# Optimization experiments

Measured on AMD Instinct MI355X. Metric: run time of the kernel, lower is better.

The kernel has to match this reference:

```python
import jax, jax.numpy as jnp
import numpy as np

N_NODES = 50000
N_EDGES = 800000
IN_CH = 128
CH = 128
OUT_CH = 128
N_TAPS = 3
N_LAYERS = 2


def setup_inputs() -> dict:
    key = jax.random.key(0)
    ks = jax.random.split(key, 8)
    s = 0.05
    x = jax.random.normal(ks[0], (N_NODES, IN_CH), dtype=jnp.float32)
    edge_index = jax.random.randint(ks[1], (2, N_EDGES), 0, N_NODES)
    # readin MLP: 1 layer, plain_last=False -> Linear + activation
    w_in = jax.random.normal(ks[2], (IN_CH, CH), dtype=jnp.float32) * s
    b_in = jnp.zeros((CH,), jnp.float32)
    # per-layer GraphFilter taps: (n_taps+1) Linears of [CH, CH]
    taps_w = jax.random.normal(ks[3], (N_LAYERS, N_TAPS + 1, CH, CH), dtype=jnp.float32) * s
    taps_b = jax.random.normal(ks[4], (N_LAYERS, N_TAPS + 1, CH), dtype=jnp.float32) * s
    # readout MLP: 1 layer, plain_last=True -> Linear only
    w_out = jax.random.normal(ks[5], (CH, OUT_CH), dtype=jnp.float32) * s
    b_out = jnp.zeros((OUT_CH,), jnp.float32)
    return {
        "x": x,
        "edge_index": edge_index,
        "w_in": w_in,
        "b_in": b_in,
        "taps_w": taps_w,
        "taps_b": taps_b,
        "w_out": w_out,
        "b_out": b_out,
    }


def reference(x, edge_index, w_in, b_in, taps_w, taps_b, w_out, b_out):
    act = jax.nn.leaky_relu  # torch LeakyReLU default negative_slope=0.01
    src, dst = edge_index[0], edge_index[1]
    n = x.shape[0]

    # readin: Linear + act (plain_last=False)
    h = act(x @ w_in + b_in)

    n_layers, n_taps_p1 = taps_w.shape[0], taps_w.shape[1]
    for l in range(n_layers):
        # ResidualBlock: y = act(h); y = GraphFilter(y); h = h + y
        y = act(h)
        out = y @ taps_w[l, 0] + taps_b[l, 0]
        for k in range(1, n_taps_p1):
            # SimpleConv(aggr='sum'): y_i = sum_{(s->i) in E} y_s
            y = jax.ops.segment_sum(y[src], dst, num_segments=n)
            out = out + y @ taps_w[l, k] + taps_b[l, k]
        h = h + out

    # readout: Linear only (plain_last=True)
    return h @ w_out + b_out
```

## Files before the change

### kernel.cpp

```cpp
#include <hip/hip_runtime.h>

typedef unsigned int uint;
typedef unsigned short ushort;

using bf16x8 = __attribute__((ext_vector_type(8))) short;
using f32x4  = __attribute__((ext_vector_type(4))) float;
using u32x4  = __attribute__((ext_vector_type(4))) uint;

__device__ __forceinline__ float lrelu(float v) { return v > 0.f ? v : 0.01f * v; }
__device__ __forceinline__ float b2f(ushort u) { return __uint_as_float((uint)u << 16); }
__device__ __forceinline__ ushort f2b(float f) {
  uint u = __float_as_uint(f);
  u += 0x7fffu + ((u >> 16) & 1u);
  return (ushort)(u >> 16);
}

#define CSR_B 256
#define BKT_SHIFT 10
#define MAX_NB 64


template <int MODE, int K, int F32A>
__global__ __launch_bounds__(256) void gemm_mfma(
    const ushort* __restrict__ A0, const ushort* __restrict__ A1,
    const ushort* __restrict__ A2, const ushort* __restrict__ A3,
    const float* __restrict__ Xf,
    const ushort* __restrict__ Wt, const float* __restrict__ bias,
    float* __restrict__ h, ushort* __restrict__ yout, int do_act, int store_h,
    int N) {
  __shared__ ushort As[64][40];
  __shared__ ushort Bs[128][40];
  const int tid = threadIdx.x;
  const int lane = tid & 63;
  const int wave = tid >> 6;
  const int g = lane >> 4;
  const int mr = lane & 15;
  const int wr = wave >> 1;
  const int wc = wave & 1;
  const int row0 = blockIdx.x * 64;

  const ushort* Ap[4] = {A0, A1, A2, A3};

  f32x4 acc[2][4];
#pragma unroll
  for (int i = 0; i < 2; i++)
#pragma unroll
    for (int j = 0; j < 4; j++) acc[i][j] = (f32x4){0.f, 0.f, 0.f, 0.f};

#pragma unroll 4
  for (int kc = 0; kc < K; kc += 32) {
    {
      int m = tid >> 2, q = tid & 3;
      int r = row0 + m;
      if (r >= N) r = N - 1;
      if constexpr (F32A) {
        const float* xp = Xf + (size_t)r * 128 + kc + q * 8;
        f32x4 xa = *(const f32x4*)xp;
        f32x4 xb = *(const f32x4*)(xp + 4);
        union { u32x4 v; ushort u[8]; } o;
        o.u[0] = f2b(xa[0]); o.u[1] = f2b(xa[1]);
        o.u[2] = f2b(xa[2]); o.u[3] = f2b(xa[3]);
        o.u[4] = f2b(xb[0]); o.u[5] = f2b(xb[1]);
        o.u[6] = f2b(xb[2]); o.u[7] = f2b(xb[3]);
        *(u32x4*)&As[m][q * 8] = o.v;
      } else {
        int kg = kc + q * 8;
        const ushort* ap = Ap[kg >> 7] + ((size_t)((kg >> 6) & 1)) * N * 64 +
                           (size_t)r * 64 + (kg & 63);
        *(u32x4*)&As[m][q * 8] = *(const u32x4*)ap;
      }
    }
#pragma unroll
    for (int t = 0; t < 2; t++) {
      int slot = tid + t * 256;
      int n = slot >> 2, q = slot & 3;
      *(u32x4*)&Bs[n][q * 8] = *(const u32x4*)(Wt + (size_t)n * K + kc + q * 8);
    }
    __syncthreads();
    bf16x8 af[2], bf[4];
#pragma unroll
    for (int rt = 0; rt < 2; rt++) af[rt] = *(bf16x8*)&As[wr * 32 + rt * 16 + mr][g * 8];
#pragma unroll
    for (int ct = 0; ct < 4; ct++) bf[ct] = *(bf16x8*)&Bs[wc * 64 + ct * 16 + mr][g * 8];
#pragma unroll
    for (int rt = 0; rt < 2; rt++)
#pragma unroll
      for (int ct = 0; ct < 4; ct++)
        acc[rt][ct] = __builtin_amdgcn_mfma_f32_16x16x32_bf16(af[rt], bf[ct], acc[rt][ct], 0, 0, 0);
    __syncthreads();
  }

#pragma unroll
  for (int rt = 0; rt < 2; rt++) {
#pragma unroll
    for (int i = 0; i < 4; i++) {
      int R = row0 + wr * 32 + rt * 16 + g * 4 + i;
      if (R >= N) continue;
#pragma unroll
      for (int ct = 0; ct < 4; ct++) {
        int c = wc * 64 + ct * 16 + mr;
        float v = acc[rt][ct][i] + bias[c];
        size_t o = (size_t)R * 128 + c;
        size_t oy = (size_t)(c >> 6) * N * 64 + (size_t)R * 64 + (c & 63);
        if (MODE == 0) {
          float hv = lrelu(v);
          h[o] = hv;
          yout[oy] = f2b(lrelu(hv));
        } else if (MODE == 1) {
          float hv = h[o] + v;
          if (store_h) h[o] = hv;
          if (yout) yout[oy] = f2b(do_act ? lrelu(hv) : hv);
        } else {
          h[o] = v;
        }
      }
    }
  }
}

__global__ __launch_bounds__(256) void agg_bf16(const ushort* __restrict__ yin,
                                                ushort* __restrict__ yout,
                                                const int* __restrict__ rowp,
                                                const ushort* __restrict__ esrc, int N) {
  int t = threadIdx.x;
  int chunk = blockIdx.x & 1;
  int node = (blockIdx.x >> 1) * 32 + (t >> 3);
  if (node >= N) return;
  int lane = t & 7;
  const ushort* yb = yin + (size_t)chunk * N * 64 + lane * 8;
  int beg = rowp[node], end = rowp[node + 1];
  float s[8] = {0.f, 0.f, 0.f, 0.f, 0.f, 0.f, 0.f, 0.f};
  int j = beg;
  for (; j + 8 <= end; j += 8) {
    int is[8];
#pragma unroll
    for (int e = 0; e < 8; e++) is[e] = esrc[j + e];
    u32x4 w[8];
#pragma unroll
    for (int e = 0; e < 8; e++) w[e] = *(const u32x4*)(yb + (size_t)is[e] * 64);
#pragma unroll
    for (int e = 0; e < 8; e++) {
      union { u32x4 v; ushort u[8]; } q;
      q.v = w[e];
#pragma unroll
      for (int c = 0; c < 8; c++) s[c] += b2f(q.u[c]);
    }
  }
  if (j + 4 <= end) {
    int is[4];
#pragma unroll
    for (int e = 0; e < 4; e++) is[e] = esrc[j + e];
    u32x4 w[4];
#pragma unroll
    for (int e = 0; e < 4; e++) w[e] = *(const u32x4*)(yb + (size_t)is[e] * 64);
#pragma unroll
    for (int e = 0; e < 4; e++) {
      union { u32x4 v; ushort u[8]; } q;
      q.v = w[e];
#pragma unroll
      for (int c = 0; c < 8; c++) s[c] += b2f(q.u[c]);
    }
    j += 4;
  }
  for (; j < end; j++) {
    int sn = esrc[j];
    union { u32x4 v; ushort u[8]; } w;
    w.v = *(const u32x4*)(yb + (size_t)sn * 64);
#pragma unroll
    for (int e = 0; e < 8; e++) s[e] += b2f(w.u[e]);
  }
  union { u32x4 v; ushort u[8]; } o;
#pragma unroll
  for (int e = 0; e < 8; e++) o.u[e] = f2b(s[e]);
  *(u32x4*)(yout + (size_t)chunk * N * 64 + (size_t)node * 64 + lane * 8) = o.v;
}

__global__ __launch_bounds__(256) void prep_k(const float* __restrict__ w_in,
                                              const float* __restrict__ w_out,
                                              const float* __restrict__ taps_w,
                                              const float* __restrict__ taps_b,
                                              ushort* __restrict__ Wt_in,
                                              ushort* __restrict__ Wt_out,
                                              ushort* __restrict__ Wt_l0,
                                              ushort* __restrict__ Wt_l1,
                                              float* __restrict__ bsum) {
  int gid = blockIdx.x * 256 + threadIdx.x;
  if (gid < 16384) {
    int n = gid >> 7, k = gid & 127;
    Wt_in[gid] = f2b(w_in[k * 128 + n]);
  } else if (gid < 32768) {
    int i = gid - 16384;
    int n = i >> 7, k = i & 127;
    Wt_out[i] = f2b(w_out[k * 128 + n]);
  } else if (gid < 98304) {
    int i = gid - 32768;
    int n = i >> 9, k = i & 511;
    Wt_l0[i] = f2b(taps_w[(size_t)k * 128 + n]);
  } else if (gid < 163840) {
    int i = gid - 98304;
    int n = i >> 9, k = i & 511;
    Wt_l1[i] = f2b(taps_w[(size_t)(512 + k) * 128 + n]);
  } else if (gid < 164096) {
    int i = gid - 163840;
    int l = i >> 7, n = i & 127;
    float s = 0.f;
    for (int k = 0; k < 4; k++) s += taps_b[l * 512 + k * 128 + n];
    bsum[i] = s;
  }
}

__global__ __launch_bounds__(256) void chist_k(const int* __restrict__ dst,
                                               int* __restrict__ H, int E, int NB) {
  __shared__ int hh[MAX_NB];
  if (threadIdx.x < NB) hh[threadIdx.x] = 0;
  __syncthreads();
  int chunk = (E + gridDim.x - 1) / gridDim.x;
  int beg = blockIdx.x * chunk, end = min(E, beg + chunk);
  for (int e = beg + threadIdx.x; e < end; e += 256)
    atomicAdd(&hh[dst[e] >> BKT_SHIFT], 1);
  __syncthreads();
  if (threadIdx.x < NB) H[threadIdx.x * gridDim.x + blockIdx.x] = hh[threadIdx.x];
}

__global__ __launch_bounds__(256) void cscan_k(int* __restrict__ H, int M) {
  __shared__ int sm[256];
  int per = (M + 255) / 256;
  int b0 = threadIdx.x * per;
  int hi = min(M, b0 + per);
  int sum = 0;
  for (int i = b0; i < hi; i++) sum += H[i];
  sm[threadIdx.x] = sum;
  __syncthreads();
  int x = sum;
  for (int off = 1; off < 256; off <<= 1) {
    int tt = (threadIdx.x >= off) ? sm[threadIdx.x - off] : 0;
    __syncthreads();
    x += tt;
    sm[threadIdx.x] = x;
    __syncthreads();
  }
  int run = x - sum;
  for (int i = b0; i < hi; i++) {
    int v = H[i];
    H[i] = run;
    run += v;
  }
}

__global__ __launch_bounds__(256) void cscatter_k(const int* __restrict__ src,
                                                  const int* __restrict__ dst,
                                                  const int* __restrict__ H,
                                                  uint* __restrict__ packed,
                                                  int E, int NB) {
  __shared__ int cur[MAX_NB];
  int chunk = (E + gridDim.x - 1) / gridDim.x;
  int beg = blockIdx.x * chunk, end = min(E, beg + chunk);
  if (threadIdx.x < NB) cur[threadIdx.x] = H[threadIdx.x * gridDim.x + blockIdx.x];
  __syncthreads();
  for (int e = beg + threadIdx.x; e < end; e += 256) {
    int d = dst[e];
    int pos = atomicAdd(&cur[d >> BKT_SHIFT], 1);
    packed[pos] = ((uint)d << 16) | (uint)src[e];
  }
}

__global__ __launch_bounds__(256) void fsort_k(const uint* __restrict__ packed,
                                               const int* __restrict__ H,
                                               ushort* __restrict__ esrc,
                                               int* __restrict__ rowp,
                                               int N, int E, int NB) {
  __shared__ int hist[1 << BKT_SHIFT];
  __shared__ int cur[1 << BKT_SHIFT];
  __shared__ int sm[256];
  const int bkt = blockIdx.x;
  const int base = bkt << BKT_SHIFT;
  const int nb_nodes = min(1 << BKT_SHIFT, N - base);
  const int start = H[bkt * CSR_B];
  const int end = (bkt == NB - 1) ? E : H[(bkt + 1) * CSR_B];

  for (int i = threadIdx.x; i < (1 << BKT_SHIFT); i += 256) hist[i] = 0;
  __syncthreads();
  for (int e = start + threadIdx.x; e < end; e += 256)
    atomicAdd(&hist[(packed[e] >> 16) - base], 1);
  __syncthreads();

  int t4 = threadIdx.x * 4;
  int l0 = hist[t4], l1 = hist[t4 + 1], l2 = hist[t4 + 2], l3 = hist[t4 + 3];
  int ssum = l0 + l1 + l2 + l3;
  sm[threadIdx.x] = ssum;
  __syncthreads();
  int x = ssum;
  for (int off = 1; off < 256; off <<= 1) {
    int tt = (threadIdx.x >= off) ? sm[threadIdx.x - off] : 0;
    __syncthreads();
    x += tt;
    sm[threadIdx.x] = x;
    __syncthreads();
  }
  int c0 = start + x - ssum;
  int c1 = c0 + l0, c2 = c1 + l1, c3 = c2 + l2;
  cur[t4] = c0; cur[t4 + 1] = c1; cur[t4 + 2] = c2; cur[t4 + 3] = c3;
  if (t4 + 0 < nb_nodes) rowp[base + t4 + 0] = c0;
  if (t4 + 1 < nb_nodes) rowp[base + t4 + 1] = c1;
  if (t4 + 2 < nb_nodes) rowp[base + t4 + 2] = c2;
  if (t4 + 3 < nb_nodes) rowp[base + t4 + 3] = c3;
  __syncthreads();

  for (int e = start + threadIdx.x; e < end; e += 256) {
    uint p = packed[e];
    int pos = atomicAdd(&cur[(p >> 16) - base], 1);
    esrc[pos] = (ushort)(p & 0xffffu);
  }
  if (bkt == 0 && threadIdx.x == 0) rowp[N] = E;
}

extern "C" void kernel_launch(void* const* d_in, const int* in_sizes, int n_in,
                              void* d_out, int out_size, void* d_ws, size_t ws_size,
                              hipStream_t stream) {
  const float* x      = (const float*)d_in[0];
  const int*   ei     = (const int*)d_in[1];
  const float* w_in   = (const float*)d_in[2];
  const float* b_in   = (const float*)d_in[3];
  const float* taps_w = (const float*)d_in[4];
  const float* taps_b = (const float*)d_in[5];
  const float* w_out  = (const float*)d_in[6];
  const float* b_out  = (const float*)d_in[7];

  const int N = in_sizes[0] / 128;
  const int E = in_sizes[1] / 2;
  const int* src = ei;
  const int* dst = ei + E;
  const int NB = (N + (1 << BKT_SHIFT) - 1) >> BKT_SHIFT;

  float* h = (float*)d_out;

  const size_t yelem = (size_t)N * 128;
  ushort* y0 = (ushort*)d_ws;
  ushort* y1 = y0 + yelem;
  ushort* y2 = y1 + yelem;
  ushort* y3 = y2 + yelem;
  ushort* Wt_in  = y3 + yelem;
  ushort* Wt_out = Wt_in + 128 * 128;
  ushort* Wt_l0  = Wt_out + 128 * 128;
  ushort* Wt_l1  = Wt_l0 + 128 * 512;
  float*  bsum   = (float*)(Wt_l1 + 128 * 512);
  int*    rowp   = (int*)(bsum + 256);
  int*    H      = rowp + (N + 1);
  uint*   packed = (uint*)(H + MAX_NB * CSR_B);
  ushort* esrc   = (ushort*)(packed + E);

  const int gemmB = (N + 63) / 64;
  const int aggB  = ((N + 31) / 32) * 2;

  chist_k<<<CSR_B, 256, 0, stream>>>(dst, H, E, NB);
  cscan_k<<<1, 256, 0, stream>>>(H, NB * CSR_B);
  cscatter_k<<<CSR_B, 256, 0, stream>>>(src, dst, H, packed, E, NB);
  fsort_k<<<NB, 256, 0, stream>>>(packed, H, esrc, rowp, N, E, NB);

  prep_k<<<641, 256, 0, stream>>>(w_in, w_out, taps_w, taps_b,
                                  Wt_in, Wt_out, Wt_l0, Wt_l1, bsum);

  gemm_mfma<0, 128, 1><<<gemmB, 256, 0, stream>>>(
      nullptr, nullptr, nullptr, nullptr, x, Wt_in, b_in, h, y0, 0, 1, N);

  for (int l = 0; l < 2; l++) {
    const ushort* Wt_l = (l == 0) ? Wt_l0 : Wt_l1;
    agg_bf16<<<aggB, 256, 0, stream>>>(y0, y1, rowp, esrc, N);
    agg_bf16<<<aggB, 256, 0, stream>>>(y1, y2, rowp, esrc, N);
    agg_bf16<<<aggB, 256, 0, stream>>>(y2, y3, rowp, esrc, N);
    gemm_mfma<1, 512, 0><<<gemmB, 256, 0, stream>>>(
        y0, y1, y2, y3, nullptr, Wt_l, bsum + l * 128, h, y0,
        (l == 0) ? 1 : 0, (l == 0) ? 1 : 0, N);
  }

  gemm_mfma<2, 128, 0><<<gemmB, 256, 0, stream>>>(
      y0, y0, y0, y0, nullptr, Wt_out, b_out, (float*)d_out, nullptr, 0, 1, N);
}
```

Before: 383.2 us.

## Fuse third-hop aggregation into the tap GEMM prologue via shared memory

The third neighbor aggregation is moved out of its own kernel and into the layer GEMM. Each block now gathers the aggregated rows for its 64 nodes into a shared-memory tile, and the last K-chunks read their A operand from that tile. This drops one kernel launch per layer and the write and re-read of the y3 buffer. In exchange the gather runs with only one block per 64 rows and 16 threads per row. That may cut latency hiding and parallelism compared with the standalone aggregation kernel, and it uses more LDS per block.

```diff
diff --git a/kernel.cpp b/kernel.cpp
--- a/kernel.cpp
+++ b/kernel.cpp
@@ -20,16 +20,18 @@
 #define MAX_NB 64
 
 
-template <int MODE, int K, int F32A>
+template <int MODE, int K, int F32A, int FUSE>
 __global__ __launch_bounds__(256) void gemm_mfma(
     const ushort* __restrict__ A0, const ushort* __restrict__ A1,
     const ushort* __restrict__ A2, const ushort* __restrict__ A3,
     const float* __restrict__ Xf,
     const ushort* __restrict__ Wt, const float* __restrict__ bias,
+    const int* __restrict__ rowp, const ushort* __restrict__ esrc,
     float* __restrict__ h, ushort* __restrict__ yout, int do_act, int store_h,
     int N) {
   __shared__ ushort As[64][40];
   __shared__ ushort Bs[128][40];
+  __shared__ ushort Ss[FUSE ? 64 : 1][136];
   const int tid = threadIdx.x;
   const int lane = tid & 63;
   const int wave = tid >> 6;
@@ -41,6 +43,44 @@
 
   const ushort* Ap[4] = {A0, A1, A2, A3};
 
+  if constexpr (FUSE) {
+    const int lane16 = tid & 15;
+    const int chunk = lane16 >> 3;
+    const ushort* yb = A2 + (size_t)chunk * N * 64 + (lane16 & 7) * 8;
+#pragma unroll
+    for (int p = 0; p < 4; p++) {
+      int m = (tid >> 4) + p * 16;
+      int r = row0 + m;
+      if (r >= N) r = N - 1;
+      int beg = rowp[r], end = rowp[r + 1];
+      float s[8] = {0.f, 0.f, 0.f, 0.f, 0.f, 0.f, 0.f, 0.f};
+      int j = beg;
+      for (; j + 4 <= end; j += 4) {
+        int i0 = esrc[j], i1 = esrc[j + 1], i2 = esrc[j + 2], i3 = esrc[j + 3];
+        union { u32x4 v; ushort u[8]; } w0, w1, w2, w3;
+        w0.v = *(const u32x4*)(yb + (size_t)i0 * 64);
+        w1.v = *(const u32x4*)(yb + (size_t)i1 * 64);
+        w2.v = *(const u32x4*)(yb + (size_t)i2 * 64);
+        w3.v = *(const u32x4*)(yb + (size_t)i3 * 64);
+#pragma unroll
+        for (int e = 0; e < 8; e++)
+          s[e] += (b2f(w0.u[e]) + b2f(w1.u[e])) + (b2f(w2.u[e]) + b2f(w3.u[e]));
+      }
+      for (; j < end; j++) {
+        int sn = esrc[j];
+        union { u32x4 v; ushort u[8]; } w;
+        w.v = *(const u32x4*)(yb + (size_t)sn * 64);
+#pragma unroll
+        for (int e = 0; e < 8; e++) s[e] += b2f(w.u[e]);
+      }
+      union { u32x4 v; ushort u[8]; } o;
+#pragma unroll
+      for (int e = 0; e < 8; e++) o.u[e] = f2b(s[e]);
+      *(u32x4*)&Ss[m][lane16 * 8] = o.v;
+    }
+    __syncthreads();
+  }
+
   f32x4 acc[2][4];
 #pragma unroll
   for (int i = 0; i < 2; i++)
@@ -49,7 +89,7 @@
 
 #pragma unroll 4
   for (int kc = 0; kc < K; kc += 32) {
-    {
+    if (!FUSE || kc < 384) {
       int m = tid >> 2, q = tid & 3;
       int r = row0 + m;
       if (r >= N) r = N - 1;
@@ -78,8 +118,15 @@
     }
     __syncthreads();
     bf16x8 af[2], bf[4];
-#pragma unroll
-    for (int rt = 0; rt < 2; rt++) af[rt] = *(bf16x8*)&As[wr * 32 + rt * 16 + mr][g * 8];
+    if (FUSE && kc >= 384) {
+#pragma unroll
+      for (int rt = 0; rt < 2; rt++)
+        af[rt] = *(bf16x8*)&Ss[wr * 32 + rt * 16 + mr][(kc - 384) + g * 8];
+    } else {
+#pragma unroll
+      for (int rt = 0; rt < 2; rt++)
+        af[rt] = *(bf16x8*)&As[wr * 32 + rt * 16 + mr][g * 8];
+    }
 #pragma unroll
     for (int ct = 0; ct < 4; ct++) bf[ct] = *(bf16x8*)&Bs[wc * 64 + ct * 16 + mr][g * 8];
 #pragma unroll
@@ -360,19 +407,20 @@
   prep_k<<<641, 256, 0, stream>>>(w_in, w_out, taps_w, taps_b,
                                   Wt_in, Wt_out, Wt_l0, Wt_l1, bsum);
 
-  gemm_mfma<0, 128, 1><<<gemmB, 256, 0, stream>>>(
-      nullptr, nullptr, nullptr, nullptr, x, Wt_in, b_in, h, y0, 0, 1, N);
+  gemm_mfma<0, 128, 1, 0><<<gemmB, 256, 0, stream>>>(
+      nullptr, nullptr, nullptr, nullptr, x, Wt_in, b_in, nullptr, nullptr,
+      h, y0, 0, 1, N);
 
   for (int l = 0; l < 2; l++) {
     const ushort* Wt_l = (l == 0) ? Wt_l0 : Wt_l1;
     agg_bf16<<<aggB, 256, 0, stream>>>(y0, y1, rowp, esrc, N);
     agg_bf16<<<aggB, 256, 0, stream>>>(y1, y2, rowp, esrc, N);
-    agg_bf16<<<aggB, 256, 0, stream>>>(y2, y3, rowp, esrc, N);
-    gemm_mfma<1, 512, 0><<<gemmB, 256, 0, stream>>>(
-        y0, y1, y2, y3, nullptr, Wt_l, bsum + l * 128, h, y0,
+    gemm_mfma<1, 512, 0, 1><<<gemmB, 256, 0, stream>>>(
+        y0, y1, y2, y2, nullptr, Wt_l, bsum + l * 128, rowp, esrc, h, y0,
         (l == 0) ? 1 : 0, (l == 0) ? 1 : 0, N);
   }
 
-  gemm_mfma<2, 128, 0><<<gemmB, 256, 0, stream>>>(
-      y0, y0, y0, y0, nullptr, Wt_out, b_out, (float*)d_out, nullptr, 0, 1, N);
-}
+  gemm_mfma<2, 128, 0, 0><<<gemmB, 256, 0, stream>>>(
+      y0, y0, y0, y0, nullptr, Wt_out, b_out, nullptr, nullptr,
+      (float*)d_out, nullptr, 0, 1, N);
+}
```

Result: no change. 386.8 us (+0.9%).
